# Performance work log

Hardware: AMD Instinct MI355X
Metric: run time of the kernel (lower is better)

The kernel has to match this reference:

```python
import jax, jax.numpy as jnp
import numpy as np

N, E, IN, H, O, K = 50000, 800000, 256, 128, 32, 5
ALPHA, EPS = 0.1, 1e-5


def setup_inputs() -> dict:
    key = jax.random.key(0)
    ks = jax.random.split(key, 20)
    nrm = lambda k, shape, s=0.02: jax.random.normal(k, shape, dtype=jnp.float32) * s
    H2 = H // 2
    return {
        "x": jax.random.normal(ks[0], (N, IN), dtype=jnp.float32),
        "edge_index": jax.random.randint(ks[1], (2, E), 0, N),
        "edge_weight": jax.random.uniform(ks[2], (E,), dtype=jnp.float32),
        # lin1 + bn1
        "W1": nrm(ks[3], (IN, H)), "b1": jnp.zeros((H,), jnp.float32),
        "g1": jnp.ones((H,), jnp.float32), "be1": jnp.zeros((H,), jnp.float32),
        "m1": nrm(ks[4], (H,), 0.1), "v1": 1.0 + 0.1 * jax.random.uniform(ks[5], (H,), dtype=jnp.float32),
        # lin2 + bn2
        "W2": nrm(ks[6], (H, H)), "b2": jnp.zeros((H,), jnp.float32),
        "g2": jnp.ones((H,), jnp.float32), "be2": jnp.zeros((H,), jnp.float32),
        "m2": nrm(ks[7], (H,), 0.1), "v2": 1.0 + 0.1 * jax.random.uniform(ks[8], (H,), dtype=jnp.float32),
        # attention over hop outputs (K+1)
        "att": jnp.ones((K + 1,), jnp.float32) + nrm(ks[9], (K + 1,), 0.1),
        # head: Linear(H, H//2) + BN + ReLU + Linear(H//2, O)
        "W3": nrm(ks[10], (H, H2)), "b3": jnp.zeros((H2,), jnp.float32),
        "g3": jnp.ones((H2,), jnp.float32), "be3": jnp.zeros((H2,), jnp.float32),
        "m3": nrm(ks[11], (H2,), 0.1), "v3": 1.0 + 0.1 * jax.random.uniform(ks[12], (H2,), dtype=jnp.float32),
        "W4": nrm(ks[13], (H2, O)), "b4": jnp.zeros((O,), jnp.float32),
    }


def _bn(t, g, b, m, v):
    # eval-mode BatchNorm1d using running stats
    return (t - m) * (g / jnp.sqrt(v + EPS)) + b


def reference(x, edge_index, edge_weight, W1, b1, g1, be1, m1, v1,
              W2, b2, g2, be2, m2, v2, att,
              W3, b3, g3, be3, m3, v3, W4, b4):
    n = x.shape[0]
    row, col = edge_index[0], edge_index[1]

    h = jax.nn.relu(_bn(x @ W1 + b1, g1, be1, m1, v1))
    identity = h
    h = jax.nn.relu(_bn(h @ W2 + b2, g2, be2, m2, v2)) + identity

    # weighted edge normalization: out-weight sum per source node, clamped >= 1
    wsum = jnp.maximum(jax.ops.segment_sum(edge_weight, row, num_segments=n), 1.0)
    edge_norm = edge_weight / wsum[row]  # [E]

    def prop(h_in):
        # APPNP-style: K inner iterations blending toward this call's h0
        h0 = h_in
        hk = h_in
        for _ in range(K):
            msg = hk[row] * edge_norm[:, None]          # [E, H] gather + scale
            agg = jax.ops.segment_sum(msg, col, num_segments=n)  # scatter-add
            hk = (1.0 - ALPHA) * agg + ALPHA * h0
        return hk

    xs = [h]
    hc = h
    for _ in range(K):  # outer loop: att has K+1 weights
        hc = prop(hc)
        xs.append(hc)

    stacked = jnp.stack(xs, axis=-1)          # [N, H, K+1]
    w = jax.nn.softmax(att)                   # [K+1]
    fused = jnp.einsum('nhk,k->nh', stacked, w)

    hid = jax.nn.relu(_bn(fused @ W3 + b3, g3, be3, m3, v3))
    return hid @ W4 + b4
```

## Files before the change

### kernel.cpp

```cpp
#include <hip/hip_runtime.h>
#include <cstddef>
#include <cstdint>

namespace {

constexpr int N   = 50000;
constexpr int E   = 800000;
constexpr int IN  = 256;
constexpr int H   = 128;
constexpr int H2v = 64;
constexpr int O   = 32;
constexpr int K   = 5;
constexpr float ALPHA = 0.1f;
constexpr float EPS   = 1e-5f;
constexpr int NPAD = 50048;
constexpr int NPW  = 4;
constexpr int CAP  = 48;

typedef __bf16 bf16x8 __attribute__((ext_vector_type(8)));
typedef float  f32x4  __attribute__((ext_vector_type(4)));

__device__ inline uint32_t pack2_bf16(float x, float y) {
  uint32_t ux = __float_as_uint(x);
  uint32_t uy = __float_as_uint(y);
  ux = (ux + 0x7FFFu + ((ux >> 16) & 1u)) >> 16;
  uy = (uy + 0x7FFFu + ((uy >> 16) & 1u)) & 0xFFFF0000u;
  return uy | ux;
}
__device__ inline unsigned short bf16_1(float x) {
  uint32_t u = __float_as_uint(x);
  return (unsigned short)((u + 0x7FFFu + ((u >> 16) & 1u)) >> 16);
}
__device__ inline float bf16_lo(uint32_t v) { return __uint_as_float(v << 16); }
__device__ inline float bf16_hi(uint32_t v) { return __uint_as_float(v & 0xFFFF0000u); }
__device__ inline float bf16_f(unsigned short h) { return __uint_as_float(((uint32_t)h) << 16); }

__global__ void zero_init_kernel(int* __restrict__ cnt, float* __restrict__ wsum) {
  int i = blockIdx.x * blockDim.x + threadIdx.x;
  if (i < NPAD) cnt[i] = 0;
  if (i < N) wsum[i] = 0.f;
}

__global__ void softmax_att_kernel(const float* __restrict__ att, float* __restrict__ wk) {
  if (threadIdx.x == 0 && blockIdx.x == 0) {
    float mx = att[0];
    for (int i = 1; i < K + 1; ++i) mx = fmaxf(mx, att[i]);
    float ex[K + 1];
    float s = 0.f;
    for (int i = 0; i < K + 1; ++i) { ex[i] = expf(att[i] - mx); s += ex[i]; }
    for (int i = 0; i < K + 1; ++i) wk[i] = ex[i] / s;
  }
}

__global__ void fused_fill_kernel(const int* __restrict__ row, const int* __restrict__ col,
                                  const float* __restrict__ ew,
                                  int* __restrict__ cnt, float* __restrict__ wsum,
                                  uint2* __restrict__ csr) {
  int i = blockIdx.x * blockDim.x + threadIdx.x;
  if (i < E) {
    int s = row[i];
    float w = ew[i];
    atomicAdd(&wsum[s], w);
    int d = col[i];
    int old = atomicAdd(&cnt[d], 1);
    if (old < CAP) csr[(size_t)d * CAP + old] = make_uint2((uint32_t)s, __float_as_uint(w));
  }
}

__global__ __launch_bounds__(256) void normalize_kernel(const int* __restrict__ cnt,
                                                        const float* __restrict__ wsum,
                                                        uint2* __restrict__ csr) {
  int wave = threadIdx.x >> 6;
  int lane = threadIdx.x & 63;
  int node = blockIdx.x * 4 + wave;
  if (node >= N) return;
  int deg = min(cnt[node], CAP);
  if (lane < deg) {
    size_t slot = (size_t)node * CAP + lane;
    uint2 e = csr[slot];
    float w = __uint_as_float(e.y) / fmaxf(wsum[e.x], 1.0f);
    csr[slot] = make_uint2(e.x, __float_as_uint(w));
  }
}

__global__ void conv_wt_kernel(const float* __restrict__ W, unsigned short* __restrict__ Wt,
                               int Kdim) {
  int t = blockIdx.x * blockDim.x + threadIdx.x;
  int k8 = Kdim / 8;
  int n = t / k8;
  int kk = (t % k8) * 8;
  if (n >= H) return;
  float f[8];
#pragma unroll
  for (int j = 0; j < 8; ++j) f[j] = W[(size_t)(kk + j) * H + n];
  uint4 pk;
  pk.x = pack2_bf16(f[0], f[1]);
  pk.y = pack2_bf16(f[2], f[3]);
  pk.z = pack2_bf16(f[4], f[5]);
  pk.w = pack2_bf16(f[6], f[7]);
  *(uint4*)&Wt[(size_t)n * Kdim + kk] = pk;
}

__global__ __launch_bounds__(256) void mlp1_mfma_kernel(
    const float* __restrict__ x, const unsigned short* __restrict__ Wt1,
    const float* __restrict__ b1, const float* __restrict__ g1,
    const float* __restrict__ be1, const float* __restrict__ m1,
    const float* __restrict__ v1, unsigned short* __restrict__ h1bf) {
  int wave = threadIdx.x >> 6;
  int lane = threadIdx.x & 63;
  int m_base = blockIdx.x * 64 + wave * 16;
  int idx16 = lane & 15;
  int quad = lane >> 4;
  int m = m_base + idx16;
  bf16x8 afrag[8];
  if (m < N) {
    const float* xrow = x + (size_t)m * IN + quad * 8;
#pragma unroll
    for (int k0 = 0; k0 < 8; ++k0) {
      float4 a = *(const float4*)(xrow + k0 * 32);
      float4 b = *(const float4*)(xrow + k0 * 32 + 4);
      uint4 pk;
      pk.x = pack2_bf16(a.x, a.y);
      pk.y = pack2_bf16(a.z, a.w);
      pk.z = pack2_bf16(b.x, b.y);
      pk.w = pack2_bf16(b.z, b.w);
      afrag[k0] = *(bf16x8*)&pk;
    }
  } else {
    uint4 z = {0, 0, 0, 0};
#pragma unroll
    for (int k0 = 0; k0 < 8; ++k0) afrag[k0] = *(bf16x8*)&z;
  }
#pragma unroll
  for (int n0 = 0; n0 < 8; ++n0) {
    f32x4 acc = {0.f, 0.f, 0.f, 0.f};
    const unsigned short* wrow = Wt1 + (size_t)(n0 * 16 + idx16) * IN + quad * 8;
#pragma unroll
    for (int k0 = 0; k0 < 8; ++k0) {
      bf16x8 bfrag = *(const bf16x8*)(wrow + k0 * 32);
      acc = __builtin_amdgcn_mfma_f32_16x16x32_bf16(afrag[k0], bfrag, acc, 0, 0, 0);
    }
    int n = n0 * 16 + idx16;
    float sc = g1[n] * rsqrtf(v1[n] + EPS);
    float ad = b1[n] - m1[n];
    float bb = be1[n];
#pragma unroll
    for (int r = 0; r < 4; ++r) {
      int mm = m_base + quad * 4 + r;
      float val = fmaxf((acc[r] + ad) * sc + bb, 0.f);
      h1bf[(size_t)mm * H + n] = bf16_1(val);
    }
  }
}

__global__ __launch_bounds__(256) void mlp2_mfma_kernel(
    const unsigned short* __restrict__ h1bf, const unsigned short* __restrict__ Wt2,
    const float* __restrict__ b2, const float* __restrict__ g2,
    const float* __restrict__ be2, const float* __restrict__ m2,
    const float* __restrict__ v2, unsigned short* __restrict__ h0bf,
    float* __restrict__ fused, const float* __restrict__ wk) {
  int wave = threadIdx.x >> 6;
  int lane = threadIdx.x & 63;
  int m_base = blockIdx.x * 64 + wave * 16;
  int idx16 = lane & 15;
  int quad = lane >> 4;
  bf16x8 afrag[4];
  const unsigned short* arow = h1bf + (size_t)(m_base + idx16) * H + quad * 8;
#pragma unroll
  for (int k0 = 0; k0 < 4; ++k0) afrag[k0] = *(const bf16x8*)(arow + k0 * 32);
  float w0 = wk[0];
#pragma unroll
  for (int n0 = 0; n0 < 8; ++n0) {
    f32x4 acc = {0.f, 0.f, 0.f, 0.f};
    const unsigned short* wrow = Wt2 + (size_t)(n0 * 16 + idx16) * H + quad * 8;
#pragma unroll
    for (int k0 = 0; k0 < 4; ++k0) {
      bf16x8 bfrag = *(const bf16x8*)(wrow + k0 * 32);
      acc = __builtin_amdgcn_mfma_f32_16x16x32_bf16(afrag[k0], bfrag, acc, 0, 0, 0);
    }
    int n = n0 * 16 + idx16;
    float sc = g2[n] * rsqrtf(v2[n] + EPS);
    float ad = b2[n] - m2[n];
    float bb = be2[n];
#pragma unroll
    for (int r = 0; r < 4; ++r) {
      int m = m_base + quad * 4 + r;
      if (m < N) {
        float idv = bf16_f(h1bf[(size_t)m * H + n]);
        float val = fmaxf((acc[r] + ad) * sc + bb, 0.f) + idv;
        h0bf[(size_t)m * H + n] = bf16_1(val);
        fused[(size_t)m * H + n] = w0 * val;
      }
    }
  }
}

__global__ __launch_bounds__(256) void prop_kernel(
    const unsigned short* __restrict__ hk, const unsigned short* __restrict__ h0,
    unsigned short* __restrict__ outb,
    const int* __restrict__ cnt, const uint2* __restrict__ csr,
    float* __restrict__ fused, const float* __restrict__ wk, int wj) {
  int wave = threadIdx.x >> 6;
  int lane = threadIdx.x & 63;
  int quarter = lane >> 4;
  int colb = (lane & 15) * 8;
  int node0 = (blockIdx.x * 4 + wave) * NPW;
  float wj_w = (wj >= 0) ? wk[wj] : 0.f;
  for (int nn = 0; nn < NPW; ++nn) {
    int node = node0 + nn;
    int deg = min(cnt[node], CAP);
    int beg = node * CAP;
    int end = beg + deg;
    float a[8];
#pragma unroll
    for (int j = 0; j < 8; ++j) a[j] = 0.f;
    int nfull = deg >> 2;
    int qi = 0;
    for (; qi + 4 <= nfull; qi += 4) {
      uint2 ce[4];
      uint4 rv[4];
#pragma unroll
      for (int u = 0; u < 4; ++u) ce[u] = csr[beg + (qi + u) * 4 + quarter];
#pragma unroll
      for (int u = 0; u < 4; ++u) rv[u] = *(const uint4*)&hk[(size_t)ce[u].x * H + colb];
#pragma unroll
      for (int u = 0; u < 4; ++u) {
        float w = __uint_as_float(ce[u].y);
        a[0] += w * bf16_lo(rv[u].x); a[1] += w * bf16_hi(rv[u].x);
        a[2] += w * bf16_lo(rv[u].y); a[3] += w * bf16_hi(rv[u].y);
        a[4] += w * bf16_lo(rv[u].z); a[5] += w * bf16_hi(rv[u].z);
        a[6] += w * bf16_lo(rv[u].w); a[7] += w * bf16_hi(rv[u].w);
      }
    }
    for (; qi < nfull; ++qi) {
      uint2 ce = csr[beg + qi * 4 + quarter];
      uint4 rv = *(const uint4*)&hk[(size_t)ce.x * H + colb];
      float w = __uint_as_float(ce.y);
      a[0] += w * bf16_lo(rv.x); a[1] += w * bf16_hi(rv.x);
      a[2] += w * bf16_lo(rv.y); a[3] += w * bf16_hi(rv.y);
      a[4] += w * bf16_lo(rv.z); a[5] += w * bf16_hi(rv.z);
      a[6] += w * bf16_lo(rv.w); a[7] += w * bf16_hi(rv.w);
    }
    if (deg & 3) {
      int e = beg + nfull * 4 + quarter;
      bool valid = e < end;
      uint2 ce = csr[valid ? e : beg];
      float w = valid ? __uint_as_float(ce.y) : 0.f;
      uint4 rv = *(const uint4*)&hk[(size_t)ce.x * H + colb];
      a[0] += w * bf16_lo(rv.x); a[1] += w * bf16_hi(rv.x);
      a[2] += w * bf16_lo(rv.y); a[3] += w * bf16_hi(rv.y);
      a[4] += w * bf16_lo(rv.z); a[5] += w * bf16_hi(rv.z);
      a[6] += w * bf16_lo(rv.w); a[7] += w * bf16_hi(rv.w);
    }
#pragma unroll
    for (int j = 0; j < 8; ++j) {
      a[j] += __shfl_xor(a[j], 16, 64);
      a[j] += __shfl_xor(a[j], 32, 64);
    }
    size_t idx = (size_t)node * H + colb;
    if (quarter == 0) {
      uint4 hv = *(const uint4*)&h0[idx];
      float v0 = (1.f - ALPHA) * a[0] + ALPHA * bf16_lo(hv.x);
      float v1 = (1.f - ALPHA) * a[1] + ALPHA * bf16_hi(hv.x);
      float v2 = (1.f - ALPHA) * a[2] + ALPHA * bf16_lo(hv.y);
      float v3 = (1.f - ALPHA) * a[3] + ALPHA * bf16_hi(hv.y);
      float v4 = (1.f - ALPHA) * a[4] + ALPHA * bf16_lo(hv.z);
      float v5 = (1.f - ALPHA) * a[5] + ALPHA * bf16_hi(hv.z);
      float v6 = (1.f - ALPHA) * a[6] + ALPHA * bf16_lo(hv.w);
      float v7 = (1.f - ALPHA) * a[7] + ALPHA * bf16_hi(hv.w);
      uint4 pk;
      pk.x = pack2_bf16(v0, v1);
      pk.y = pack2_bf16(v2, v3);
      pk.z = pack2_bf16(v4, v5);
      pk.w = pack2_bf16(v6, v7);
      *(uint4*)&outb[idx] = pk;
    } else if (quarter == 1 && wj >= 0 && node < N) {
      uint4 hv = *(const uint4*)&h0[idx];
      float v0 = (1.f - ALPHA) * a[0] + ALPHA * bf16_lo(hv.x);
      float v1 = (1.f - ALPHA) * a[1] + ALPHA * bf16_hi(hv.x);
      float v2 = (1.f - ALPHA) * a[2] + ALPHA * bf16_lo(hv.y);
      float v3 = (1.f - ALPHA) * a[3] + ALPHA * bf16_hi(hv.y);
      float v4 = (1.f - ALPHA) * a[4] + ALPHA * bf16_lo(hv.z);
      float v5 = (1.f - ALPHA) * a[5] + ALPHA * bf16_hi(hv.z);
      float v6 = (1.f - ALPHA) * a[6] + ALPHA * bf16_lo(hv.w);
      float v7 = (1.f - ALPHA) * a[7] + ALPHA * bf16_hi(hv.w);
      float4 f0 = *(float4*)&fused[idx];
      float4 f1 = *(float4*)&fused[idx + 4];
      f0.x += wj_w * v0; f0.y += wj_w * v1; f0.z += wj_w * v2; f0.w += wj_w * v3;
      f1.x += wj_w * v4; f1.y += wj_w * v5; f1.z += wj_w * v6; f1.w += wj_w * v7;
      *(float4*)&fused[idx] = f0;
      *(float4*)&fused[idx + 4] = f1;
    }
  }
}

__global__ __launch_bounds__(64) void head_kernel(
    const float* __restrict__ fused, const float* __restrict__ W3,
    const float* __restrict__ b3, const float* __restrict__ g3,
    const float* __restrict__ be3, const float* __restrict__ m3,
    const float* __restrict__ v3, const float* __restrict__ W4,
    const float* __restrict__ b4, float* __restrict__ out) {
  __shared__ float fl[16][H];
  __shared__ float hl[16][H2v];
  int node0 = blockIdx.x * 16;
  int t = threadIdx.x;
  for (int idx = t * 4; idx < 16 * H; idx += 64 * 4) {
    int r = idx >> 7, c = idx & (H - 1);
    *(float4*)&fl[r][c] = *(const float4*)&fused[(size_t)(node0 + r) * H + c];
  }
  __syncthreads();
  {
    int ng = t >> 4;
    int c0 = (t & 15) * 4;
    float acc[4][4];
#pragma unroll
    for (int a = 0; a < 4; ++a)
#pragma unroll
      for (int b = 0; b < 4; ++b) acc[a][b] = 0.f;
    for (int k = 0; k < H; k += 4) {
      float4 xv[4];
#pragma unroll
      for (int a = 0; a < 4; ++a) xv[a] = *(const float4*)&fl[ng * 4 + a][k];
      float4 wv[4];
#pragma unroll
      for (int j = 0; j < 4; ++j) wv[j] = *(const float4*)&W3[(size_t)(k + j) * H2v + c0];
#pragma unroll
      for (int a = 0; a < 4; ++a) {
        float xa0 = xv[a].x, xa1 = xv[a].y, xa2 = xv[a].z, xa3 = xv[a].w;
        acc[a][0] += xa0 * wv[0].x + xa1 * wv[1].x + xa2 * wv[2].x + xa3 * wv[3].x;
        acc[a][1] += xa0 * wv[0].y + xa1 * wv[1].y + xa2 * wv[2].y + xa3 * wv[3].y;
        acc[a][2] += xa0 * wv[0].z + xa1 * wv[1].z + xa2 * wv[2].z + xa3 * wv[3].z;
        acc[a][3] += xa0 * wv[0].w + xa1 * wv[1].w + xa2 * wv[2].w + xa3 * wv[3].w;
      }
    }
    float sc[4], ad[4], bb[4];
#pragma unroll
    for (int b = 0; b < 4; ++b) {
      int c = c0 + b;
      sc[b] = g3[c] * rsqrtf(v3[c] + EPS);
      ad[b] = b3[c] - m3[c];
      bb[b] = be3[c];
    }
#pragma unroll
    for (int a = 0; a < 4; ++a)
#pragma unroll
      for (int b = 0; b < 4; ++b)
        hl[ng * 4 + a][c0 + b] = fmaxf((acc[a][b] + ad[b]) * sc[b] + bb[b], 0.f);
  }
  __syncthreads();
  {
    int co = t & 31;
    int nh = t >> 5;
    float bias = b4[co];
#pragma unroll
    for (int a = 0; a < 8; ++a) {
      int nloc = nh * 8 + a;
      float accf = bias;
      for (int k = 0; k < H2v; k += 4) {
        float4 hv = *(const float4*)&hl[nloc][k];
        accf += hv.x * W4[(size_t)(k + 0) * O + co];
        accf += hv.y * W4[(size_t)(k + 1) * O + co];
        accf += hv.z * W4[(size_t)(k + 2) * O + co];
        accf += hv.w * W4[(size_t)(k + 3) * O + co];
      }
      out[(size_t)(node0 + nloc) * O + co] = accf;
    }
  }
}

}

extern "C" void kernel_launch(void* const* d_in, const int* in_sizes, int n_in,
                              void* d_out, int out_size, void* d_ws, size_t ws_size,
                              hipStream_t stream) {
  const float* x   = (const float*)d_in[0];
  const int*   ei  = (const int*)d_in[1];
  const float* ew  = (const float*)d_in[2];
  const float* W1  = (const float*)d_in[3];
  const float* b1  = (const float*)d_in[4];
  const float* g1  = (const float*)d_in[5];
  const float* be1 = (const float*)d_in[6];
  const float* m1  = (const float*)d_in[7];
  const float* v1  = (const float*)d_in[8];
  const float* W2  = (const float*)d_in[9];
  const float* b2  = (const float*)d_in[10];
  const float* g2  = (const float*)d_in[11];
  const float* be2 = (const float*)d_in[12];
  const float* m2  = (const float*)d_in[13];
  const float* v2  = (const float*)d_in[14];
  const float* att = (const float*)d_in[15];
  const float* W3  = (const float*)d_in[16];
  const float* b3  = (const float*)d_in[17];
  const float* g3  = (const float*)d_in[18];
  const float* be3 = (const float*)d_in[19];
  const float* m3  = (const float*)d_in[20];
  const float* v3  = (const float*)d_in[21];
  const float* W4  = (const float*)d_in[22];
  const float* b4  = (const float*)d_in[23];
  const int* row = ei;
  const int* col = ei + E;
  float* out = (float*)d_out;

  char* p = (char*)d_ws;
  auto carve = [&](size_t bytes) -> void* {
    void* q = (void*)p;
    p += (bytes + 255) & ~(size_t)255;
    return q;
  };
  int*   cnt     = (int*)carve((size_t)NPAD * 4);
  float* wsum    = (float*)carve((size_t)N * 4);
  uint2* csr     = (uint2*)carve((size_t)N * CAP * 8);
  float* wk      = (float*)carve(64);
  unsigned short* Wt1  = (unsigned short*)carve((size_t)H * IN * 2);
  unsigned short* Wt2  = (unsigned short*)carve((size_t)H * H * 2);
  unsigned short* h1bf = (unsigned short*)carve((size_t)NPAD * H * 2);
  unsigned short* bf0  = (unsigned short*)carve((size_t)NPAD * H * 2);
  unsigned short* bfA  = (unsigned short*)carve((size_t)NPAD * H * 2);
  unsigned short* bfB  = (unsigned short*)carve((size_t)NPAD * H * 2);
  float* fused   = (float*)carve((size_t)N * H * 4);

  const int tb = 256;
  zero_init_kernel<<<(NPAD + tb - 1) / tb, tb, 0, stream>>>(cnt, wsum);
  softmax_att_kernel<<<1, 64, 0, stream>>>(att, wk);
  fused_fill_kernel<<<(E + tb - 1) / tb, tb, 0, stream>>>(row, col, ew, cnt, wsum, csr);
  normalize_kernel<<<(N + 3) / 4, 256, 0, stream>>>(cnt, wsum, csr);

  conv_wt_kernel<<<(H * (IN / 8) + tb - 1) / tb, tb, 0, stream>>>(W1, Wt1, IN);
  conv_wt_kernel<<<(H * (H / 8) + tb - 1) / tb, tb, 0, stream>>>(W2, Wt2, H);

  mlp1_mfma_kernel<<<NPAD / 64, 256, 0, stream>>>(x, Wt1, b1, g1, be1, m1, v1, h1bf);
  mlp2_mfma_kernel<<<NPAD / 64, 256, 0, stream>>>(h1bf, Wt2, b2, g2, be2, m2, v2,
                                                  bf0, fused, wk);

  unsigned short* h0 = bf0;
  unsigned short* pa = bfA;
  unsigned short* pb = bfB;
  const int prop_blocks = NPAD / (4 * NPW);
  for (int j = 1; j <= K; ++j) {
    const unsigned short* src = h0;
    unsigned short* dst = pa;
    for (int i = 0; i < K; ++i) {
      int wj = (i == K - 1) ? j : -1;
      prop_kernel<<<prop_blocks, 256, 0, stream>>>(src, h0, dst, cnt, csr, fused, wk, wj);
      if (i < K - 1) {
        src = dst;
        dst = (dst == pa) ? pb : pa;
      }
    }
    unsigned short* oldh0 = h0;
    h0 = pa;
    pa = pb;
    pb = oldh0;
  }

  head_kernel<<<N / 16, 64, 0, stream>>>(fused, W3, b3, g3, be3, m3, v3, W4, b4, out);
}
```

Baseline: 1.222 ms.

## Bucket edges by source quarter and co-schedule gathers across nodes in prop

The normalize step now sorts each node's edge list into four buckets by source-node range and stores bucket boundaries in a per-node meta word. The prop kernel has each wave own 13 nodes and walk the buckets in lockstep, with a block barrier between buckets, so concurrent gathers touch a narrower slice of the feature matrix and hit cache more often. Gathers now use half-wave 8-byte loads instead of quarter-wave 16-byte loads. The fill/mlp1 and normalize/mlp2 pairs and the init/softmax pair are merged into shared launches to cut launch count. In exchange the prop kernel holds a large register accumulator array, and edge-weight accumulation order changes.

```diff
diff --git a/kernel.cpp b/kernel.cpp
--- a/kernel.cpp
+++ b/kernel.cpp
@@ -14,8 +14,13 @@
 constexpr float ALPHA = 0.1f;
 constexpr float EPS   = 1e-5f;
 constexpr int NPAD = 50048;
-constexpr int NPW  = 4;
 constexpr int CAP  = 48;
+constexpr int Q1 = 12500, Q2 = 25000, Q3 = 37500;
+constexpr int PROP_BLOCKS = 1024;
+constexpr int NPW = 13;
+constexpr int FILL_BLOCKS = (E + 255) / 256;
+constexpr int MLP_BLOCKS  = NPAD / 64;
+constexpr int NORM_BLOCKS = NPAD / 4;
 
 typedef __bf16 bf16x8 __attribute__((ext_vector_type(8)));
 typedef float  f32x4  __attribute__((ext_vector_type(4)));
@@ -35,51 +40,18 @@
 __device__ inline float bf16_hi(uint32_t v) { return __uint_as_float(v & 0xFFFF0000u); }
 __device__ inline float bf16_f(unsigned short h) { return __uint_as_float(((uint32_t)h) << 16); }
 
-__global__ void zero_init_kernel(int* __restrict__ cnt, float* __restrict__ wsum) {
+__global__ void init_kernel(int* __restrict__ cnt, float* __restrict__ wsum,
+                            const float* __restrict__ att, float* __restrict__ wk) {
   int i = blockIdx.x * blockDim.x + threadIdx.x;
   if (i < NPAD) cnt[i] = 0;
   if (i < N) wsum[i] = 0.f;
-}
-
-__global__ void softmax_att_kernel(const float* __restrict__ att, float* __restrict__ wk) {
-  if (threadIdx.x == 0 && blockIdx.x == 0) {
+  if (i == 0) {
     float mx = att[0];
-    for (int i = 1; i < K + 1; ++i) mx = fmaxf(mx, att[i]);
+    for (int j = 1; j < K + 1; ++j) mx = fmaxf(mx, att[j]);
     float ex[K + 1];
     float s = 0.f;
-    for (int i = 0; i < K + 1; ++i) { ex[i] = expf(att[i] - mx); s += ex[i]; }
-    for (int i = 0; i < K + 1; ++i) wk[i] = ex[i] / s;
-  }
-}
-
-__global__ void fused_fill_kernel(const int* __restrict__ row, const int* __restrict__ col,
-                                  const float* __restrict__ ew,
-                                  int* __restrict__ cnt, float* __restrict__ wsum,
-                                  uint2* __restrict__ csr) {
-  int i = blockIdx.x * blockDim.x + threadIdx.x;
-  if (i < E) {
-    int s = row[i];
-    float w = ew[i];
-    atomicAdd(&wsum[s], w);
-    int d = col[i];
-    int old = atomicAdd(&cnt[d], 1);
-    if (old < CAP) csr[(size_t)d * CAP + old] = make_uint2((uint32_t)s, __float_as_uint(w));
-  }
-}
-
-__global__ __launch_bounds__(256) void normalize_kernel(const int* __restrict__ cnt,
-                                                        const float* __restrict__ wsum,
-                                                        uint2* __restrict__ csr) {
-  int wave = threadIdx.x >> 6;
-  int lane = threadIdx.x & 63;
-  int node = blockIdx.x * 4 + wave;
-  if (node >= N) return;
-  int deg = min(cnt[node], CAP);
-  if (lane < deg) {
-    size_t slot = (size_t)node * CAP + lane;
-    uint2 e = csr[slot];
-    float w = __uint_as_float(e.y) / fmaxf(wsum[e.x], 1.0f);
-    csr[slot] = make_uint2(e.x, __float_as_uint(w));
+    for (int j = 0; j < K + 1; ++j) { ex[j] = expf(att[j] - mx); s += ex[j]; }
+    for (int j = 0; j < K + 1; ++j) wk[j] = ex[j] / s;
   }
 }
 
@@ -101,14 +73,29 @@
   *(uint4*)&Wt[(size_t)n * Kdim + kk] = pk;
 }
 
-__global__ __launch_bounds__(256) void mlp1_mfma_kernel(
-    const float* __restrict__ x, const unsigned short* __restrict__ Wt1,
-    const float* __restrict__ b1, const float* __restrict__ g1,
-    const float* __restrict__ be1, const float* __restrict__ m1,
-    const float* __restrict__ v1, unsigned short* __restrict__ h1bf) {
+
+__device__ void fill_body(int bid, const int* __restrict__ row, const int* __restrict__ col,
+                          const float* __restrict__ ew, int* __restrict__ cnt,
+                          float* __restrict__ wsum, uint2* __restrict__ csr) {
+  int i = bid * 256 + (int)threadIdx.x;
+  if (i < E) {
+    int s = row[i];
+    float w = ew[i];
+    atomicAdd(&wsum[s], w);
+    int d = col[i];
+    int old = atomicAdd(&cnt[d], 1);
+    if (old < CAP) csr[(size_t)d * CAP + old] = make_uint2((uint32_t)s, __float_as_uint(w));
+  }
+}
+
+__device__ void mlp1_body(int bid, const float* __restrict__ x,
+                          const unsigned short* __restrict__ Wt1,
+                          const float* __restrict__ b1, const float* __restrict__ g1,
+                          const float* __restrict__ be1, const float* __restrict__ m1,
+                          const float* __restrict__ v1, unsigned short* __restrict__ h1bf) {
   int wave = threadIdx.x >> 6;
   int lane = threadIdx.x & 63;
-  int m_base = blockIdx.x * 64 + wave * 16;
+  int m_base = bid * 64 + wave * 16;
   int idx16 = lane & 15;
   int quad = lane >> 4;
   int m = m_base + idx16;
@@ -153,15 +140,66 @@
   }
 }
 
-__global__ __launch_bounds__(256) void mlp2_mfma_kernel(
-    const unsigned short* __restrict__ h1bf, const unsigned short* __restrict__ Wt2,
-    const float* __restrict__ b2, const float* __restrict__ g2,
-    const float* __restrict__ be2, const float* __restrict__ m2,
-    const float* __restrict__ v2, unsigned short* __restrict__ h0bf,
-    float* __restrict__ fused, const float* __restrict__ wk) {
+__global__ __launch_bounds__(256) void fill_mlp1_kernel(
+    const int* __restrict__ row, const int* __restrict__ col, const float* __restrict__ ew,
+    int* __restrict__ cnt, float* __restrict__ wsum, uint2* __restrict__ csr,
+    const float* __restrict__ x, const unsigned short* __restrict__ Wt1,
+    const float* __restrict__ b1, const float* __restrict__ g1,
+    const float* __restrict__ be1, const float* __restrict__ m1,
+    const float* __restrict__ v1, unsigned short* __restrict__ h1bf) {
+  if ((int)blockIdx.x < FILL_BLOCKS)
+    fill_body(blockIdx.x, row, col, ew, cnt, wsum, csr);
+  else
+    mlp1_body(blockIdx.x - FILL_BLOCKS, x, Wt1, b1, g1, be1, m1, v1, h1bf);
+}
+
+__device__ void norm_body(int bid, const int* __restrict__ cnt, const float* __restrict__ wsum,
+                          uint2* __restrict__ csr, uint32_t* __restrict__ meta) {
   int wave = threadIdx.x >> 6;
   int lane = threadIdx.x & 63;
-  int m_base = blockIdx.x * 64 + wave * 16;
+  int node = bid * 4 + wave;
+  if (node >= NPAD) return;
+  if (node >= N) {
+    if (lane == 0) meta[node] = 0;
+    return;
+  }
+  int deg = min(cnt[node], CAP);
+  size_t base = (size_t)node * CAP;
+  bool act = lane < deg;
+  uint2 e = make_uint2(0u, 0u);
+  float w = 0.f;
+  int b = 4;
+  if (act) {
+    e = csr[base + lane];
+    w = __uint_as_float(e.y) / fmaxf(wsum[e.x], 1.0f);
+    int s = (int)e.x;
+    b = (s >= Q1) + (s >= Q2) + (s >= Q3);
+  }
+  unsigned long long below = (lane == 63) ? ~0ull >> 1 : ((1ull << lane) - 1ull);
+  below = (1ull << lane) - 1ull;
+  int cum = 0;
+  int pos = 0;
+  uint32_t mv = 0;
+#pragma unroll
+  for (int bb = 0; bb < 4; ++bb) {
+    unsigned long long m = __ballot(act && b == bb);
+    if (act && b == bb) pos = cum + (int)__popcll(m & below);
+    cum += (int)__popcll(m);
+    mv |= ((uint32_t)cum) << (8 * bb);
+  }
+  if (act) csr[base + pos] = make_uint2(e.x, __float_as_uint(w));
+  if (lane == 0) meta[node] = mv;
+}
+
+__device__ void mlp2_body(int bid, const unsigned short* __restrict__ h1bf,
+                          const unsigned short* __restrict__ Wt2,
+                          const float* __restrict__ b2, const float* __restrict__ g2,
+                          const float* __restrict__ be2, const float* __restrict__ m2,
+                          const float* __restrict__ v2, unsigned short* __restrict__ h0bf,
+                          float* __restrict__ fused, const float* __restrict__ wk) {
+  int wave = threadIdx.x >> 6;
+  int lane = threadIdx.x & 63;
+  int m_base = bid * 64 + wave * 16;
   int idx16 = lane & 15;
   int quad = lane >> 4;
   bf16x8 afrag[4];
@@ -195,101 +233,94 @@
   }
 }
 
-__global__ __launch_bounds__(256) void prop_kernel(
+__global__ __launch_bounds__(256) void norm_mlp2_kernel(
+    const int* __restrict__ cnt, const float* __restrict__ wsum,
+    uint2* __restrict__ csr, uint32_t* __restrict__ meta,
+    const unsigned short* __restrict__ h1bf, const unsigned short* __restrict__ Wt2,
+    const float* __restrict__ b2, const float* __restrict__ g2,
+    const float* __restrict__ be2, const float* __restrict__ m2,
+    const float* __restrict__ v2, unsigned short* __restrict__ h0bf,
+    float* __restrict__ fused, const float* __restrict__ wk) {
+  if ((int)blockIdx.x < NORM_BLOCKS)
+    norm_body(blockIdx.x, cnt, wsum, csr, meta);
+  else
+    mlp2_body(blockIdx.x - NORM_BLOCKS, h1bf, Wt2, b2, g2, be2, m2, v2, h0bf, fused, wk);
+}
+
+__global__ __launch_bounds__(256, 4) void prop_kernel(
     const unsigned short* __restrict__ hk, const unsigned short* __restrict__ h0,
     unsigned short* __restrict__ outb,
-    const int* __restrict__ cnt, const uint2* __restrict__ csr,
+    const uint32_t* __restrict__ meta, const uint2* __restrict__ csr,
     float* __restrict__ fused, const float* __restrict__ wk, int wj) {
   int wave = threadIdx.x >> 6;
   int lane = threadIdx.x & 63;
-  int quarter = lane >> 4;
-  int colb = (lane & 15) * 8;
-  int node0 = (blockIdx.x * 4 + wave) * NPW;
+  int half = lane >> 5;
+  int hl = lane & 31;
+  int gwave = blockIdx.x * 4 + wave;
+  int base_node = gwave * NPW;
+  float acc[NPW][4];
+#pragma unroll
+  for (int nn = 0; nn < NPW; ++nn)
+#pragma unroll
+    for (int j = 0; j < 4; ++j) acc[nn][j] = 0.f;
+  uint32_t mv[NPW];
+#pragma unroll
+  for (int nn = 0; nn < NPW; ++nn) {
+    int node = base_node + nn;
+    mv[nn] = (node < NPAD) ? meta[node] : 0u;
+  }
+#pragma unroll
+  for (int c = 0; c < 4; ++c) {
+#pragma unroll
+    for (int nn = 0; nn < NPW; ++nn) {
+      int node = base_node + nn;
+      if (node >= NPAD) continue;
+      int st = (c == 0) ? 0 : (int)((mv[nn] >> (8 * (c - 1))) & 255u);
+      int en = (int)((mv[nn] >> (8 * c)) & 255u);
+      size_t mbase = (size_t)node * CAP;
+      int ng = (en - st + 1) >> 1;
+      for (int g = 0; g < ng; ++g) {
+        int e = st + g * 2 + half;
+        bool v = e < en;
+        uint2 ce = csr[mbase + (v ? e : st)];
+        float w = v ? __uint_as_float(ce.y) : 0.f;
+        uint2 rv = *(const uint2*)&hk[(size_t)ce.x * H + hl * 4];
+        acc[nn][0] += w * bf16_lo(rv.x);
+        acc[nn][1] += w * bf16_hi(rv.x);
+        acc[nn][2] += w * bf16_lo(rv.y);
+        acc[nn][3] += w * bf16_hi(rv.y);
+      }
+    }
+    __syncthreads();
+  }
   float wj_w = (wj >= 0) ? wk[wj] : 0.f;
+#pragma unroll
   for (int nn = 0; nn < NPW; ++nn) {
-    int node = node0 + nn;
-    int deg = min(cnt[node], CAP);
-    int beg = node * CAP;
-    int end = beg + deg;
-    float a[8];
-#pragma unroll
-    for (int j = 0; j < 8; ++j) a[j] = 0.f;
-    int nfull = deg >> 2;
-    int qi = 0;
-    for (; qi + 4 <= nfull; qi += 4) {
-      uint2 ce[4];
-      uint4 rv[4];
-#pragma unroll
-      for (int u = 0; u < 4; ++u) ce[u] = csr[beg + (qi + u) * 4 + quarter];
-#pragma unroll
-      for (int u = 0; u < 4; ++u) rv[u] = *(const uint4*)&hk[(size_t)ce[u].x * H + colb];
-#pragma unroll
-      for (int u = 0; u < 4; ++u) {
-        float w = __uint_as_float(ce[u].y);
-        a[0] += w * bf16_lo(rv[u].x); a[1] += w * bf16_hi(rv[u].x);
-        a[2] += w * bf16_lo(rv[u].y); a[3] += w * bf16_hi(rv[u].y);
-        a[4] += w * bf16_lo(rv[u].z); a[5] += w * bf16_hi(rv[u].z);
-        a[6] += w * bf16_lo(rv[u].w); a[7] += w * bf16_hi(rv[u].w);
-      }
-    }
-    for (; qi < nfull; ++qi) {
-      uint2 ce = csr[beg + qi * 4 + quarter];
-      uint4 rv = *(const uint4*)&hk[(size_t)ce.x * H + colb];
-      float w = __uint_as_float(ce.y);
-      a[0] += w * bf16_lo(rv.x); a[1] += w * bf16_hi(rv.x);
-      a[2] += w * bf16_lo(rv.y); a[3] += w * bf16_hi(rv.y);
-      a[4] += w * bf16_lo(rv.z); a[5] += w * bf16_hi(rv.z);
-      a[6] += w * bf16_lo(rv.w); a[7] += w * bf16_hi(rv.w);
-    }
-    if (deg & 3) {
-      int e = beg + nfull * 4 + quarter;
-      bool valid = e < end;
-      uint2 ce = csr[valid ? e : beg];
-      float w = valid ? __uint_as_float(ce.y) : 0.f;
-      uint4 rv = *(const uint4*)&hk[(size_t)ce.x * H + colb];
-      a[0] += w * bf16_lo(rv.x); a[1] += w * bf16_hi(rv.x);
-      a[2] += w * bf16_lo(rv.y); a[3] += w * bf16_hi(rv.y);
-      a[4] += w * bf16_lo(rv.z); a[5] += w * bf16_hi(rv.z);
-      a[6] += w * bf16_lo(rv.w); a[7] += w * bf16_hi(rv.w);
-    }
-#pragma unroll
-    for (int j = 0; j < 8; ++j) {
-      a[j] += __shfl_xor(a[j], 16, 64);
-      a[j] += __shfl_xor(a[j], 32, 64);
-    }
-    size_t idx = (size_t)node * H + colb;
-    if (quarter == 0) {
-      uint4 hv = *(const uint4*)&h0[idx];
-      float v0 = (1.f - ALPHA) * a[0] + ALPHA * bf16_lo(hv.x);
-      float v1 = (1.f - ALPHA) * a[1] + ALPHA * bf16_hi(hv.x);
-      float v2 = (1.f - ALPHA) * a[2] + ALPHA * bf16_lo(hv.y);
-      float v3 = (1.f - ALPHA) * a[3] + ALPHA * bf16_hi(hv.y);
-      float v4 = (1.f - ALPHA) * a[4] + ALPHA * bf16_lo(hv.z);
-      float v5 = (1.f - ALPHA) * a[5] + ALPHA * bf16_hi(hv.z);
-      float v6 = (1.f - ALPHA) * a[6] + ALPHA * bf16_lo(hv.w);
-      float v7 = (1.f - ALPHA) * a[7] + ALPHA * bf16_hi(hv.w);
-      uint4 pk;
+    int node = base_node + nn;
+    if (node >= N) continue;
+    float a[4];
+#pragma unroll
+    for (int j = 0; j < 4; ++j) {
+      a[j] = acc[nn][j] + __shfl_xor(acc[nn][j], 32, 64);
+    }
+    size_t idx = (size_t)node * H + hl * 4;
+    uint2 hv = *(const uint2*)&h0[idx];
+    float v0 = (1.f - ALPHA) * a[0] + ALPHA * bf16_lo(hv.x);
+    float v1 = (1.f - ALPHA) * a[1] + ALPHA * bf16_hi(hv.x);
+    float v2 = (1.f - ALPHA) * a[2] + ALPHA * bf16_lo(hv.y);
+    float v3 = (1.f - ALPHA) * a[3] + ALPHA * bf16_hi(hv.y);
+    if (half == 0) {
+      uint2 pk;
       pk.x = pack2_bf16(v0, v1);
       pk.y = pack2_bf16(v2, v3);
-      pk.z = pack2_bf16(v4, v5);
-      pk.w = pack2_bf16(v6, v7);
-      *(uint4*)&outb[idx] = pk;
-    } else if (quarter == 1 && wj >= 0 && node < N) {
-      uint4 hv = *(const uint4*)&h0[idx];
-      float v0 = (1.f - ALPHA) * a[0] + ALPHA * bf16_lo(hv.x);
-      float v1 = (1.f - ALPHA) * a[1] + ALPHA * bf16_hi(hv.x);
-      float v2 = (1.f - ALPHA) * a[2] + ALPHA * bf16_lo(hv.y);
-      float v3 = (1.f - ALPHA) * a[3] + ALPHA * bf16_hi(hv.y);
-      float v4 = (1.f - ALPHA) * a[4] + ALPHA * bf16_lo(hv.z);
-      float v5 = (1.f - ALPHA) * a[5] + ALPHA * bf16_hi(hv.z);
-      float v6 = (1.f - ALPHA) * a[6] + ALPHA * bf16_lo(hv.w);
-      float v7 = (1.f - ALPHA) * a[7] + ALPHA * bf16_hi(hv.w);
-      float4 f0 = *(float4*)&fused[idx];
-      float4 f1 = *(float4*)&fused[idx + 4];
-      f0.x += wj_w * v0; f0.y += wj_w * v1; f0.z += wj_w * v2; f0.w += wj_w * v3;
-      f1.x += wj_w * v4; f1.y += wj_w * v5; f1.z += wj_w * v6; f1.w += wj_w * v7;
-      *(float4*)&fused[idx] = f0;
-      *(float4*)&fused[idx + 4] = f1;
+      *(uint2*)&outb[idx] = pk;
+    } else if (wj >= 0) {
+      float4 f = *(float4*)&fused[idx];
+      f.x += wj_w * v0;
+      f.y += wj_w * v1;
+      f.z += wj_w * v2;
+      f.w += wj_w * v3;
+      *(float4*)&fused[idx] = f;
     }
   }
 }
@@ -407,41 +438,38 @@
     p += (bytes + 255) & ~(size_t)255;
     return q;
   };
-  int*   cnt     = (int*)carve((size_t)NPAD * 4);
-  float* wsum    = (float*)carve((size_t)N * 4);
-  uint2* csr     = (uint2*)carve((size_t)N * CAP * 8);
-  float* wk      = (float*)carve(64);
+  int*      cnt  = (int*)carve((size_t)NPAD * 4);
+  float*    wsum = (float*)carve((size_t)N * 4);
+  uint32_t* meta = (uint32_t*)carve((size_t)NPAD * 4);
+  uint2*    csr  = (uint2*)carve((size_t)N * CAP * 8);
+  float*    wk   = (float*)carve(64);
   unsigned short* Wt1  = (unsigned short*)carve((size_t)H * IN * 2);
   unsigned short* Wt2  = (unsigned short*)carve((size_t)H * H * 2);
   unsigned short* h1bf = (unsigned short*)carve((size_t)NPAD * H * 2);
   unsigned short* bf0  = (unsigned short*)carve((size_t)NPAD * H * 2);
   unsigned short* bfA  = (unsigned short*)carve((size_t)NPAD * H * 2);
   unsigned short* bfB  = (unsigned short*)carve((size_t)NPAD * H * 2);
-  float* fused   = (float*)carve((size_t)N * H * 4);
+  float* fused = (float*)carve((size_t)N * H * 4);
 
   const int tb = 256;
-  zero_init_kernel<<<(NPAD + tb - 1) / tb, tb, 0, stream>>>(cnt, wsum);
-  softmax_att_kernel<<<1, 64, 0, stream>>>(att, wk);
-  fused_fill_kernel<<<(E + tb - 1) / tb, tb, 0, stream>>>(row, col, ew, cnt, wsum, csr);
-  normalize_kernel<<<(N + 3) / 4, 256, 0, stream>>>(cnt, wsum, csr);
-
+  init_kernel<<<(NPAD + tb - 1) / tb, tb, 0, stream>>>(cnt, wsum, att, wk);
   conv_wt_kernel<<<(H * (IN / 8) + tb - 1) / tb, tb, 0, stream>>>(W1, Wt1, IN);
   conv_wt_kernel<<<(H * (H / 8) + tb - 1) / tb, tb, 0, stream>>>(W2, Wt2, H);
 
-  mlp1_mfma_kernel<<<NPAD / 64, 256, 0, stream>>>(x, Wt1, b1, g1, be1, m1, v1, h1bf);
-  mlp2_mfma_kernel<<<NPAD / 64, 256, 0, stream>>>(h1bf, Wt2, b2, g2, be2, m2, v2,
-                                                  bf0, fused, wk);
+  fill_mlp1_kernel<<<FILL_BLOCKS + MLP_BLOCKS, 256, 0, stream>>>(
+      row, col, ew, cnt, wsum, csr, x, Wt1, b1, g1, be1, m1, v1, h1bf);
+  norm_mlp2_kernel<<<NORM_BLOCKS + MLP_BLOCKS, 256, 0, stream>>>(
+      cnt, wsum, csr, meta, h1bf, Wt2, b2, g2, be2, m2, v2, bf0, fused, wk);
 
   unsigned short* h0 = bf0;
   unsigned short* pa = bfA;
   unsigned short* pb = bfB;
-  const int prop_blocks = NPAD / (4 * NPW);
   for (int j = 1; j <= K; ++j) {
     const unsigned short* src = h0;
     unsigned short* dst = pa;
     for (int i = 0; i < K; ++i) {
       int wj = (i == K - 1) ? j : -1;
-      prop_kernel<<<prop_blocks, 256, 0, stream>>>(src, h0, dst, cnt, csr, fused, wk, wj);
+      prop_kernel<<<PROP_BLOCKS, 256, 0, stream>>>(src, h0, dst, meta, csr, fused, wk, wj);
       if (i < K - 1) {
         src = dst;
         dst = (dst == pa) ? pb : pa;
```

New measurement: 2.729 ms. +123.3%, slower.
